# Optimization experiments

Measured on AMD Instinct MI355X. Metric: run time of the kernel, lower is better.

Reference implementation:

```python
import jax, jax.numpy as jnp
import numpy as np

N_NODES = 100000
N_EDGES = 800000
IN_DIM = 128
OUT_DIM = 128


def setup_inputs() -> dict:
    key = jax.random.key(0)
    k_h, k_w, k_src, k_dst = jax.random.split(key, 4)
    h = jax.random.normal(k_h, (N_NODES, IN_DIM), dtype=jnp.float32)
    # xavier_normal_ with relu gain ~ sqrt(2) * sqrt(2/(fan_in+fan_out))
    gain = np.sqrt(2.0)
    std = gain * np.sqrt(2.0 / (IN_DIM + OUT_DIM))
    W = jax.random.normal(k_w, (OUT_DIM, IN_DIM), dtype=jnp.float32) * std
    src = jax.random.randint(k_src, (N_EDGES,), 0, N_NODES, dtype=jnp.int64)
    dst = jax.random.randint(k_dst, (N_EDGES,), 0, N_NODES, dtype=jnp.int64)
    return {"h": h, "W": W, "src": src, "dst": dst}


def reference(h, W, src, dst):
    # fc + ReLU is applied per-edge to the gathered src feature, then summed
    # over incoming edges per dst node. Since fc acts on src features only,
    # project once per node ([N, in] @ [in, out]) then gather per edge.
    proj = jax.nn.relu(jnp.matmul(h, W.T))          # [N, out_dim]
    msgs = proj[src]                                 # [E, out_dim] (gather)
    out = jax.ops.segment_sum(msgs, dst, num_segments=N_NODES)  # [N, out_dim]
    return out
```

## Files before the change

### kernel.cpp

```cpp
#include <hip/hip_runtime.h>
#include <hip/hip_bf16.h>

#define IN_DIM 128
#define OUT_DIM 128
#define CAP 32

typedef __attribute__((ext_vector_type(8))) short short8;
typedef __attribute__((ext_vector_type(8))) unsigned short ushort8;
typedef __attribute__((ext_vector_type(4))) float floatx4;

__device__ __forceinline__ unsigned short f2bf(float x) {
    union { float f; unsigned int u; } a; a.f = x;
    unsigned int u = a.u;
    unsigned int r = (u + 0x7fffu + ((u >> 16) & 1u)) >> 16;
    return (unsigned short)r;
}
__device__ __forceinline__ ushort2 f2bf2(float x, float y) {
    __hip_bfloat162 h2 = __float22bfloat162_rn(make_float2(x, y));
    union { __hip_bfloat162 h; ushort2 u; } c; c.h = h2; return c.u;
}
__device__ __forceinline__ float bf_lo(unsigned int v) {
    union { unsigned int u; float f; } a; a.u = v << 16; return a.f;
}
__device__ __forceinline__ float bf_hi(unsigned int v) {
    union { unsigned int u; float f; } a; a.u = v & 0xffff0000u; return a.f;
}

#define APAD 136

__global__ __launch_bounds__(256) void prep_kernel(const float* __restrict__ W,
                                                   unsigned short* __restrict__ Wb,
                                                   int* __restrict__ counts,
                                                   int M, int nz) {
    if ((int)blockIdx.x < nz) {
        int i = blockIdx.x * 256 + threadIdx.x;
        if (i < M) counts[i] = 0;
    } else {
#pragma unroll
        for (int q = 0; q < 8; q++) {
            int g = q * 256 + threadIdx.x;
            int fragid = g >> 6;
            int lane   = g & 63;
            int nt = fragid >> 2, ks = fragid & 3;
            int row = nt * 16 + (lane & 15);
            int col = ks * 32 + (lane >> 4) * 8;
            const float* s = &W[(size_t)row * IN_DIM + col];
            float4 v0 = *(const float4*)s;
            float4 v1 = *(const float4*)(s + 4);
            ushort2 ab = f2bf2(v0.x, v0.y), cd = f2bf2(v0.z, v0.w);
            ushort2 ef = f2bf2(v1.x, v1.y), gh = f2bf2(v1.z, v1.w);
            ushort8 o;
            o[0] = ab.x; o[1] = ab.y; o[2] = cd.x; o[3] = cd.y;
            o[4] = ef.x; o[5] = ef.y; o[6] = gh.x; o[7] = gh.y;
            *(ushort8*)&Wb[(size_t)g * 8] = o;
        }
    }
}

__global__ __launch_bounds__(256, 5) void fused_proj_bucket(
    const float* __restrict__ h, const unsigned short* __restrict__ Wb,
    unsigned short* __restrict__ projb,
    const int* __restrict__ src, const int* __restrict__ dst,
    int* __restrict__ counts, int* __restrict__ edges,
    int M, int E)
{
    __shared__ unsigned short As[64][APAD];

    const int t    = threadIdx.x;
    const int wave = t >> 6;
    const int lane = t & 63;
    const int block_m = blockIdx.x * 64;
    const int gtid = blockIdx.x * 256 + t;
    const int T    = gridDim.x * 256;

    int e0 = gtid, e1 = gtid + T;
    int d0 = 0, d1 = 0, s0 = 0, s1 = 0, p0 = CAP, p1 = CAP;
    const bool v0 = e0 < E, v1 = e1 < E;
    if (v0) { d0 = dst[e0]; s0 = src[e0]; }
    if (v1) { d1 = dst[e1]; s1 = src[e1]; }
    if (v0) p0 = atomicAdd(&counts[d0], 1);
    if (v1) p1 = atomicAdd(&counts[d1], 1);

#pragma unroll
    for (int p = 0; p < 8; p++) {
        int c = p * 256 + t;
        int row = c >> 5;
        int ch  = c & 31;
        int gm = block_m + row;
        float4 v = make_float4(0.f, 0.f, 0.f, 0.f);
        if (gm < M) v = *(const float4*)&h[(size_t)gm * IN_DIM + ch * 4];
        ushort2 lo = f2bf2(v.x, v.y), hi = f2bf2(v.z, v.w);
        ushort4 b; b.x = lo.x; b.y = lo.y; b.z = hi.x; b.w = hi.y;
        *(ushort4*)&As[row][ch * 4] = b;
    }

    __syncthreads();

    const int mrow = wave * 16 + (lane & 15);
    const int kq   = (lane >> 4) * 8;
    floatx4 acc[8] = {};

#pragma unroll
    for (int ks = 0; ks < 4; ks++) {
        short8 a = *(const short8*)&As[mrow][ks * 32 + kq];
#pragma unroll
        for (int nt = 0; nt < 8; nt++) {
            short8 b = *(const short8*)&Wb[(size_t)((nt * 4 + ks) * 64 + lane) * 8];
            acc[nt] = __builtin_amdgcn_mfma_f32_16x16x32_bf16(a, b, acc[nt], 0, 0, 0);
        }
    }

    __syncthreads();
    {
        const int rloc = wave * 16 + (lane >> 4) * 4;
        const int col  = lane & 15;
#pragma unroll
        for (int nt = 0; nt < 8; nt++)
#pragma unroll
            for (int i = 0; i < 4; i++)
                As[rloc + i][nt * 16 + col] = f2bf(fmaxf(acc[nt][i], 0.f));
    }
    __syncthreads();
#pragma unroll
    for (int q = 0; q < 4; q++) {
        int c = q * 256 + t;
        int row = c >> 4;
        int ch  = c & 15;
        int gm = block_m + row;
        if (gm < M) {
            ushort8 v = *(const ushort8*)&As[row][ch * 8];
            *(ushort8*)&projb[(size_t)gm * OUT_DIM + ch * 8] = v;
        }
    }

    if (v0 && p0 < CAP) edges[d0 * CAP + p0] = s0;
    if (v1 && p1 < CAP) edges[d1 * CAP + p1] = s1;
    for (int e = gtid + 2 * T; e < E; e += T) {
        int d = dst[e];
        int pos = atomicAdd(&counts[d], 1);
        if (pos < CAP) edges[d * CAP + pos] = src[e];
    }
}

__global__ __launch_bounds__(256) void gather_kernel(const unsigned short* __restrict__ projb,
                                                     const int* __restrict__ edges,
                                                     const int* __restrict__ counts,
                                                     float* __restrict__ out, int M) {
    const int node = blockIdx.x * 4 + (threadIdx.x >> 6);
    const int lane = threadIdx.x & 63;
    if (node >= M) return;

    int cnt = counts[node];
    if (cnt > CAP) cnt = CAP;
    const int beg = node * CAP;
    const unsigned int* base = (const unsigned int*)projb;

    float a0 = 0.f, a1 = 0.f;
    int i = 0;
    for (; i + 4 <= cnt; i += 4) {
        int s0 = edges[beg + i + 0];
        int s1 = edges[beg + i + 1];
        int s2 = edges[beg + i + 2];
        int s3 = edges[beg + i + 3];
        unsigned int w0 = base[(size_t)s0 * 64 + lane];
        unsigned int w1 = base[(size_t)s1 * 64 + lane];
        unsigned int w2 = base[(size_t)s2 * 64 + lane];
        unsigned int w3 = base[(size_t)s3 * 64 + lane];
        a0 += bf_lo(w0); a1 += bf_hi(w0);
        a0 += bf_lo(w1); a1 += bf_hi(w1);
        a0 += bf_lo(w2); a1 += bf_hi(w2);
        a0 += bf_lo(w3); a1 += bf_hi(w3);
    }
    for (; i < cnt; i++) {
        int s = edges[beg + i];
        unsigned int w = base[(size_t)s * 64 + lane];
        a0 += bf_lo(w); a1 += bf_hi(w);
    }

    *(float2*)&out[(size_t)node * OUT_DIM + lane * 2] = make_float2(a0, a1);
}

extern "C" void kernel_launch(void* const* d_in, const int* in_sizes, int n_in,
                              void* d_out, int out_size, void* d_ws, size_t ws_size,
                              hipStream_t stream) {
    const float* h   = (const float*)d_in[0];
    const float* W   = (const float*)d_in[1];
    const int*   src = (const int*)d_in[2];
    const int*   dst = (const int*)d_in[3];
    float* out = (float*)d_out;

    const int M = in_sizes[0] / IN_DIM;
    const int E = in_sizes[2];

    char* ws = (char*)d_ws;
    unsigned short* projb = (unsigned short*)ws;
    size_t off = (size_t)M * OUT_DIM * sizeof(unsigned short);
    off = (off + 255) & ~(size_t)255;
    int* counts = (int*)(ws + off);  off += (size_t)M * sizeof(int);
    off = (off + 255) & ~(size_t)255;
    int* edges  = (int*)(ws + off);  off += (size_t)M * CAP * sizeof(int);
    off = (off + 255) & ~(size_t)255;
    unsigned short* Wb = (unsigned short*)(ws + off);  off += 32 * 1024;

    const int nz = (M + 255) / 256;

    prep_kernel<<<nz + 1, 256, 0, stream>>>(W, Wb, counts, M, nz);

    fused_proj_bucket<<<(M + 63) / 64, 256, 0, stream>>>(h, Wb, projb, src, dst,
                                                         counts, edges, M, E);

    gather_kernel<<<(M + 3) / 4, 256, 0, stream>>>(projb, edges, counts, out, M);
}
```

Baseline: 205.6 us.

## Replace per-node atomic bucketing with two-level bin scatter and LDS-local CSR build

Edges are now bucketed by destination into coarse bins of 256 nodes. A block-local histogram and prefix scan write them coalesced into per-bin arrays, replacing per-edge global atomics on a per-node count array. The gather kernel then builds per-node source lists for its bin in LDS via shared atomics and a scan, and reduces projected rows one wave per node. The projection is split into its own kernel, so the edge bucketing no longer overlaps with the matmul. This adds a kernel launch, and fixed capacities (4096 edges per bin, 4608 LDS list entries) could drop edges on skewed inputs.

Result: faster. 181.8 us (-11.6%).

```diff
diff --git a/kernel.cpp b/kernel.cpp
--- a/kernel.cpp
+++ b/kernel.cpp
@@ -3,7 +3,11 @@
 
 #define IN_DIM 128
 #define OUT_DIM 128
-#define CAP 32
+
+#define BIN_SHIFT 8
+#define MAXBINS 512
+#define BIN_CAP 4096
+#define LISTS_CAP 4608
 
 typedef __attribute__((ext_vector_type(8))) short short8;
 typedef __attribute__((ext_vector_type(8))) unsigned short ushort8;
@@ -26,15 +30,13 @@
     union { unsigned int u; float f; } a; a.u = v & 0xffff0000u; return a.f;
 }
 
-#define APAD 136
-
 __global__ __launch_bounds__(256) void prep_kernel(const float* __restrict__ W,
                                                    unsigned short* __restrict__ Wb,
-                                                   int* __restrict__ counts,
-                                                   int M, int nz) {
+                                                   int* __restrict__ gcount,
+                                                   int nbins, int nz) {
     if ((int)blockIdx.x < nz) {
         int i = blockIdx.x * 256 + threadIdx.x;
-        if (i < M) counts[i] = 0;
+        if (i < nbins) gcount[i] = 0;
     } else {
 #pragma unroll
         for (int q = 0; q < 8; q++) {
@@ -57,12 +59,85 @@
     }
 }
 
-__global__ __launch_bounds__(256, 5) void fused_proj_bucket(
+__global__ __launch_bounds__(1024) void binscatter_kernel(
+    const int* __restrict__ src, const int* __restrict__ dst,
+    int* __restrict__ gcount, unsigned long long* __restrict__ binarr,
+    int E, int nbins)
+{
+    __shared__ unsigned long long stage[4096];
+    __shared__ unsigned short binof[4096];
+    __shared__ int hist[MAXBINS];
+    __shared__ int lbase[MAXBINS];
+    __shared__ int gbase[MAXBINS];
+
+    const int t = threadIdx.x;
+    const int lane = t & 63;
+    const int wave = t >> 6;
+    const int e0 = blockIdx.x * 4096;
+    const int tot = min(4096, E - e0);
+
+    for (int b = t; b < nbins; b += 1024) hist[b] = 0;
+    __syncthreads();
+
+    int myBin[4], myPos[4], mySrc[4], myDst[4];
+#pragma unroll
+    for (int k = 0; k < 4; k++) {
+        int idx = e0 + k * 1024 + t;
+        myBin[k] = -1;
+        if (idx < E) {
+            int s = src[idx];
+            int d = dst[idx];
+            int b = d >> BIN_SHIFT;
+            mySrc[k] = s; myDst[k] = d; myBin[k] = b;
+            myPos[k] = atomicAdd(&hist[b], 1);
+        }
+    }
+    __syncthreads();
+
+    for (int b = t; b < nbins; b += 1024) {
+        int c = hist[b];
+        gbase[b] = c ? atomicAdd(&gcount[b], c) : 0;
+    }
+    if (wave == 0) {
+        int run = 0;
+        for (int c = 0; c < nbins; c += 64) {
+            int idx = c + lane;
+            int h = (idx < nbins) ? hist[idx] : 0;
+            int v = h;
+#pragma unroll
+            for (int d = 1; d < 64; d <<= 1) {
+                int o = __shfl_up(v, d, 64);
+                if (lane >= d) v += o;
+            }
+            if (idx < nbins) lbase[idx] = run + v - h;
+            run += __shfl(v, 63, 64);
+        }
+    }
+    __syncthreads();
+
+#pragma unroll
+    for (int k = 0; k < 4; k++) {
+        if (myBin[k] >= 0) {
+            int slot = lbase[myBin[k]] + myPos[k];
+            stage[slot] = ((unsigned long long)(unsigned int)myDst[k] << 32) |
+                          (unsigned int)mySrc[k];
+            binof[slot] = (unsigned short)myBin[k];
+        }
+    }
+    __syncthreads();
+
+    for (int sIdx = t; sIdx < tot; sIdx += 1024) {
+        int b = binof[sIdx];
+        int gpos = gbase[b] + (sIdx - lbase[b]);
+        if (gpos < BIN_CAP)
+            binarr[(size_t)b * BIN_CAP + gpos] = stage[sIdx];
+    }
+}
+
+#define APAD 136
+__global__ __launch_bounds__(256) void proj_kernel(
     const float* __restrict__ h, const unsigned short* __restrict__ Wb,
-    unsigned short* __restrict__ projb,
-    const int* __restrict__ src, const int* __restrict__ dst,
-    int* __restrict__ counts, int* __restrict__ edges,
-    int M, int E)
+    unsigned short* __restrict__ projb, int M)
 {
     __shared__ unsigned short As[64][APAD];
 
@@ -70,16 +145,6 @@
     const int wave = t >> 6;
     const int lane = t & 63;
     const int block_m = blockIdx.x * 64;
-    const int gtid = blockIdx.x * 256 + t;
-    const int T    = gridDim.x * 256;
-
-    int e0 = gtid, e1 = gtid + T;
-    int d0 = 0, d1 = 0, s0 = 0, s1 = 0, p0 = CAP, p1 = CAP;
-    const bool v0 = e0 < E, v1 = e1 < E;
-    if (v0) { d0 = dst[e0]; s0 = src[e0]; }
-    if (v1) { d1 = dst[e1]; s1 = src[e1]; }
-    if (v0) p0 = atomicAdd(&counts[d0], 1);
-    if (v1) p1 = atomicAdd(&counts[d1], 1);
 
 #pragma unroll
     for (int p = 0; p < 8; p++) {
@@ -93,7 +158,6 @@
         ushort4 b; b.x = lo.x; b.y = lo.y; b.z = hi.x; b.w = hi.y;
         *(ushort4*)&As[row][ch * 4] = b;
     }
-
     __syncthreads();
 
     const int mrow = wave * 16 + (lane & 15);
@@ -132,52 +196,88 @@
             *(ushort8*)&projb[(size_t)gm * OUT_DIM + ch * 8] = v;
         }
     }
-
-    if (v0 && p0 < CAP) edges[d0 * CAP + p0] = s0;
-    if (v1 && p1 < CAP) edges[d1 * CAP + p1] = s1;
-    for (int e = gtid + 2 * T; e < E; e += T) {
-        int d = dst[e];
-        int pos = atomicAdd(&counts[d], 1);
-        if (pos < CAP) edges[d * CAP + pos] = src[e];
-    }
-}
-
-__global__ __launch_bounds__(256) void gather_kernel(const unsigned short* __restrict__ projb,
-                                                     const int* __restrict__ edges,
-                                                     const int* __restrict__ counts,
-                                                     float* __restrict__ out, int M) {
-    const int node = blockIdx.x * 4 + (threadIdx.x >> 6);
-    const int lane = threadIdx.x & 63;
-    if (node >= M) return;
-
-    int cnt = counts[node];
-    if (cnt > CAP) cnt = CAP;
-    const int beg = node * CAP;
+}
+
+__global__ __launch_bounds__(512) void gather_kernel(
+    const unsigned short* __restrict__ projb,
+    const unsigned long long* __restrict__ binarr,
+    const int* __restrict__ gcount,
+    float* __restrict__ out, int M)
+{
+    __shared__ int cnt[256];
+    __shared__ int base2[256];
+    __shared__ int lists[LISTS_CAP];
+
+    const int t = threadIdx.x;
+    const int lane = t & 63;
+    const int wave = t >> 6;
+    const int bin = blockIdx.x;
+    const int lo = bin << BIN_SHIFT;
+    const int nNodes = min(256, M - lo);
+    const int nE = min(gcount[bin], BIN_CAP);
+    const unsigned long long* ep = &binarr[(size_t)bin * BIN_CAP];
+
+    if (t < 256) cnt[t] = 0;
+    __syncthreads();
+
+    for (int i = t; i < nE; i += 512) {
+        int n = (int)(ep[i] >> 32) & 255;
+        atomicAdd(&cnt[n], 1);
+    }
+    __syncthreads();
+
+    if (wave == 0) {
+        int run = 0;
+#pragma unroll
+        for (int c = 0; c < 256; c += 64) {
+            int h = cnt[c + lane];
+            int v = h;
+#pragma unroll
+            for (int d = 1; d < 64; d <<= 1) {
+                int o = __shfl_up(v, d, 64);
+                if (lane >= d) v += o;
+            }
+            base2[c + lane] = run + v - h;
+            run += __shfl(v, 63, 64);
+        }
+    }
+    __syncthreads();
+
+    for (int i = t; i < nE; i += 512) {
+        unsigned long long e = ep[i];
+        int n = (int)(e >> 32) & 255;
+        int pos = atomicAdd(&base2[n], 1);
+        if (pos < LISTS_CAP) lists[pos] = (int)(unsigned int)e;
+    }
+    __syncthreads();
+
     const unsigned int* base = (const unsigned int*)projb;
-
-    float a0 = 0.f, a1 = 0.f;
-    int i = 0;
-    for (; i + 4 <= cnt; i += 4) {
-        int s0 = edges[beg + i + 0];
-        int s1 = edges[beg + i + 1];
-        int s2 = edges[beg + i + 2];
-        int s3 = edges[beg + i + 3];
-        unsigned int w0 = base[(size_t)s0 * 64 + lane];
-        unsigned int w1 = base[(size_t)s1 * 64 + lane];
-        unsigned int w2 = base[(size_t)s2 * 64 + lane];
-        unsigned int w3 = base[(size_t)s3 * 64 + lane];
-        a0 += bf_lo(w0); a1 += bf_hi(w0);
-        a0 += bf_lo(w1); a1 += bf_hi(w1);
-        a0 += bf_lo(w2); a1 += bf_hi(w2);
-        a0 += bf_lo(w3); a1 += bf_hi(w3);
-    }
-    for (; i < cnt; i++) {
-        int s = edges[beg + i];
-        unsigned int w = base[(size_t)s * 64 + lane];
-        a0 += bf_lo(w); a1 += bf_hi(w);
-    }
-
-    *(float2*)&out[(size_t)node * OUT_DIM + lane * 2] = make_float2(a0, a1);
+    for (int n = wave; n < nNodes; n += 8) {
+        int c = cnt[n];
+        int st = base2[n] - c;
+        float a0 = 0.f, a1 = 0.f;
+        int i = 0;
+        for (; i + 4 <= c; i += 4) {
+            int s0 = lists[st + i + 0];
+            int s1 = lists[st + i + 1];
+            int s2 = lists[st + i + 2];
+            int s3 = lists[st + i + 3];
+            unsigned int w0 = base[(size_t)s0 * 64 + lane];
+            unsigned int w1 = base[(size_t)s1 * 64 + lane];
+            unsigned int w2 = base[(size_t)s2 * 64 + lane];
+            unsigned int w3 = base[(size_t)s3 * 64 + lane];
+            a0 += bf_lo(w0); a1 += bf_hi(w0);
+            a0 += bf_lo(w1); a1 += bf_hi(w1);
+            a0 += bf_lo(w2); a1 += bf_hi(w2);
+            a0 += bf_lo(w3); a1 += bf_hi(w3);
+        }
+        for (; i < c; i++) {
+            int s = lists[st + i];
+            unsigned int w = base[(size_t)s * 64 + lane];
+            a0 += bf_lo(w); a1 += bf_hi(w);
+        }
+        *(float2*)&out[(size_t)(lo + n) * OUT_DIM + lane * 2] = make_float2(a0, a1);
+    }
 }
 
 extern "C" void kernel_launch(void* const* d_in, const int* in_sizes, int n_in,
@@ -191,23 +291,27 @@
 
     const int M = in_sizes[0] / IN_DIM;
     const int E = in_sizes[2];
+    const int NBINS = (M + 255) >> BIN_SHIFT;
 
     char* ws = (char*)d_ws;
     unsigned short* projb = (unsigned short*)ws;
     size_t off = (size_t)M * OUT_DIM * sizeof(unsigned short);
     off = (off + 255) & ~(size_t)255;
-    int* counts = (int*)(ws + off);  off += (size_t)M * sizeof(int);
+    int* gcount = (int*)(ws + off);  off += (size_t)NBINS * sizeof(int);
     off = (off + 255) & ~(size_t)255;
-    int* edges  = (int*)(ws + off);  off += (size_t)M * CAP * sizeof(int);
+    unsigned long long* binarr = (unsigned long long*)(ws + off);
+    off += (size_t)NBINS * BIN_CAP * sizeof(unsigned long long);
     off = (off + 255) & ~(size_t)255;
     unsigned short* Wb = (unsigned short*)(ws + off);  off += 32 * 1024;
 
-    const int nz = (M + 255) / 256;
-
-    prep_kernel<<<nz + 1, 256, 0, stream>>>(W, Wb, counts, M, nz);
-
-    fused_proj_bucket<<<(M + 63) / 64, 256, 0, stream>>>(h, Wb, projb, src, dst,
-                                                         counts, edges, M, E);
-
-    gather_kernel<<<(M + 3) / 4, 256, 0, stream>>>(projb, edges, counts, out, M);
-}
+    const int nz = (NBINS + 255) / 256;
+
+    prep_kernel<<<nz + 1, 256, 0, stream>>>(W, Wb, gcount, NBINS, nz);
+
+    binscatter_kernel<<<(E + 4095) / 4096, 1024, 0, stream>>>(src, dst, gcount,
+                                                              binarr, E, NBINS);
+
+    proj_kernel<<<(M + 63) / 64, 256, 0, stream>>>(h, Wb, projb, M);
+
+    gather_kernel<<<NBINS, 512, 0, stream>>>(projb, binarr, gcount, out, M);
+}
```
